# Kernel optimization log

Measured on AMD Instinct MI355X. Metric: run time of the kernel, lower is better.

The kernel has to match this reference:

```python
import jax, jax.numpy as jnp
import numpy as np

NUM_CODES = 4096
EMBED_DIM = 64
BETA = 0.25


def setup_inputs() -> dict:
    key = jax.random.key(0)
    k1, k2 = jax.random.split(key)
    z = jax.random.normal(k1, (8, EMBED_DIM, 64, 64), dtype=jnp.float32)
    weight = jax.random.normal(k2, (NUM_CODES, EMBED_DIM), dtype=jnp.float32)
    return {"z": z, "weight": weight}


def reference(z, weight):
    # z: [B, C, H, W] -> [B, H, W, C]
    z_bhwc = jnp.moveaxis(z, 1, -1)
    z_flat = z_bhwc.reshape(-1, EMBED_DIM)  # [N, d]

    # squared-euclidean distances: ||z||^2 + ||w||^2 - 2 z.w  -> [N, num_codes]
    distance = (
        jnp.sum(z_flat ** 2, axis=1, keepdims=True)
        + jnp.sum(weight ** 2, axis=1)
        - 2.0 * jnp.einsum('bd,nd->bn', z_flat, weight)
    )
    encoding_indices = jnp.argmin(distance, axis=1)  # [N]

    # codebook lookup (gather)
    z_q = weight[encoding_indices].reshape(z_bhwc.shape)  # [B, H, W, C]

    encodings = jax.nn.one_hot(encoding_indices, NUM_CODES, dtype=z.dtype)  # [N, num_codes]
    avg_probs = jnp.mean(encodings, axis=0)
    tiny = 1e-10  # max(1e-10, finfo(fp32).tiny)
    perplexity = jnp.exp(-jnp.sum(avg_probs * jnp.log(avg_probs + tiny)))

    # commitment loss (z_q detached) — eval path, no EMA state update
    loss = BETA * jnp.mean((jax.lax.stop_gradient(z_q) - z_bhwc) ** 2)

    # straight-through estimator
    z_q = z_bhwc + jax.lax.stop_gradient(z_q - z_bhwc)
    z_q = jnp.moveaxis(z_q, -1, 1)  # back to [B, C, H, W]

    return z_q, loss, perplexity, encodings, encoding_indices
```

## Files before the change

### kernel.cpp

```cpp
#include <hip/hip_runtime.h>
#include <math.h>
#include <float.h>

#define ZQ_OFF   0
#define LOSS_OFF 2097152
#define PERP_OFF 2097153
#define ENC_OFF  2097154
#define IDX_OFF  136314882ULL
#define BETA     0.25f


__global__ void vq_wnorm(const float* __restrict__ w, float* __restrict__ wnorm) {
    int c = blockIdx.x * 256 + threadIdx.x;
    const float4* w4 = (const float4*)(w + ((size_t)c << 6));
    float s = 0.f;
    #pragma unroll
    for (int k = 0; k < 16; ++k) { float4 v = w4[k]; s += v.x*v.x + v.y*v.y + v.z*v.z + v.w*v.w; }
    wnorm[c] = s;
}

__global__ __launch_bounds__(256, 2) void vq_main(
    const float* __restrict__ z, const float* __restrict__ w,
    const float* __restrict__ wnorm, float* __restrict__ out,
    float* __restrict__ loss_ws, int* __restrict__ ticket, int* __restrict__ hist)
{
    __shared__ float zD[64][64];
    __shared__ float wl[256 * 36];
    __shared__ int   s_widx[64];
    __shared__ int   s_flag;

    const int tx   = threadIdx.x;
    const int tcol = tx & 31;
    const int trow = tx >> 5;
    const int base = blockIdx.x * 64;
    const int bb   = base >> 12;
    const int hh   = (base & 4095) >> 6;

    #pragma unroll
    for (int j = 0; j < 4; ++j) {
        int f4 = j * 256 + tx;
        int d  = f4 >> 4, w4i = f4 & 15;
        float4 v = *(const float4*)(z + (((size_t)bb * 64 + d) * 64 + hh) * 64 + w4i * 4);
        *(float4*)&zD[d][w4i * 4] = v;
    }

    float best[8]; int bidx[8];
    #pragma unroll
    for (int i = 0; i < 8; ++i) { best[i] = FLT_MAX; bidx[i] = 0; }

    float* enc = out + ENC_OFF;

    for (int ch = 0; ch < 16; ++ch) {
        const int cbase = ch << 8;
        float wn[8];
        #pragma unroll
        for (int k = 0; k < 8; ++k) wn[k] = wnorm[cbase + tcol + 32 * k];

        float acc[8][8];
        #pragma unroll
        for (int i = 0; i < 8; ++i)
            #pragma unroll
            for (int k = 0; k < 8; ++k) acc[i][k] = 0.f;

        #pragma unroll
        for (int s = 0; s < 2; ++s) {
            __syncthreads();
            #pragma unroll
            for (int j = 0; j < 8; ++j) {
                int f4 = j * 256 + tx;
                int c  = f4 >> 3, q = f4 & 7;
                float4 v = ((const float4*)w)[(size_t)(cbase + c) * 16 + s * 8 + q];
                *(float4*)&wl[c * 36 + q * 4] = v;
            }
            #pragma unroll
            for (int j = 0; j < 16; ++j) {
                int f2 = ((ch * 2 + s) * 16 + j) * 256 + tx;
                int r  = f2 >> 11, c2 = f2 & 2047;
                *((float2*)(enc + ((size_t)(base + r) << 12)) + c2) = make_float2(0.f, 0.f);
            }
            __syncthreads();

            #pragma unroll
            for (int dg = 0; dg < 8; ++dg) {
                const int d0 = s * 32 + dg * 4;
                float4 zv0[4], zv1[4];
                #pragma unroll
                for (int e = 0; e < 4; ++e) {
                    zv0[e] = *(const float4*)&zD[d0 + e][trow * 8];
                    zv1[e] = *(const float4*)&zD[d0 + e][trow * 8 + 4];
                }
                float4 wv[8];
                #pragma unroll
                for (int k = 0; k < 8; ++k)
                    wv[k] = *(const float4*)&wl[(tcol + 32 * k) * 36 + dg * 4];
                #pragma unroll
                for (int k = 0; k < 8; ++k) {
                    #pragma unroll
                    for (int e = 0; e < 4; ++e) {
                        const float wf = (e == 0) ? wv[k].x : (e == 1) ? wv[k].y
                                        : (e == 2) ? wv[k].z : wv[k].w;
                        acc[0][k] = fmaf(zv0[e].x, wf, acc[0][k]);
                        acc[1][k] = fmaf(zv0[e].y, wf, acc[1][k]);
                        acc[2][k] = fmaf(zv0[e].z, wf, acc[2][k]);
                        acc[3][k] = fmaf(zv0[e].w, wf, acc[3][k]);
                        acc[4][k] = fmaf(zv1[e].x, wf, acc[4][k]);
                        acc[5][k] = fmaf(zv1[e].y, wf, acc[5][k]);
                        acc[6][k] = fmaf(zv1[e].z, wf, acc[6][k]);
                        acc[7][k] = fmaf(zv1[e].w, wf, acc[7][k]);
                    }
                }
            }
        }

        #pragma unroll
        for (int i = 0; i < 8; ++i) {
            #pragma unroll
            for (int k = 0; k < 8; ++k) {
                float sc = fmaf(-2.f, acc[i][k], wn[k]);
                if (sc < best[i]) { best[i] = sc; bidx[i] = cbase + tcol + 32 * k; }
            }
        }
    }

    __syncthreads();
    float2* red = (float2*)wl;
    #pragma unroll
    for (int i = 0; i < 8; ++i)
        red[(trow * 8 + i) * 32 + tcol] = make_float2(best[i], __int_as_float(bidx[i]));
    __syncthreads();

    if (tx < 64) {
        float b = FLT_MAX; int bi = 0x7fffffff;
        for (int c = 0; c < 32; ++c) {
            float2 v = red[tx * 32 + c];
            int vi = __float_as_int(v.y);
            if (v.x < b || (v.x == b && vi < bi)) { b = v.x; bi = vi; }
        }
        s_widx[tx] = bi;
        out[IDX_OFF + (size_t)(base + tx)] = (float)bi;
        atomicAdd(&hist[bi], 1);
        enc[((size_t)(base + tx) << 12) + bi] = 1.0f;
    }
    __syncthreads();

    {
        const int row = tx & 63;
        const int dg  = tx >> 6;
        const int wi  = s_widx[row];
        const float* qrow = w + ((size_t)wi << 6);
        float lsum = 0.f;
        #pragma unroll
        for (int dd = 0; dd < 16; ++dd) {
            int d = dg * 16 + dd;
            float q  = qrow[d];
            float zv = zD[d][row];
            float diff = q - zv;
            lsum += diff * diff;
            out[ZQ_OFF + (((size_t)bb * 64 + d) * 64 + hh) * 64 + row] = zv + (q - zv);
        }
        #pragma unroll
        for (int off = 32; off > 0; off >>= 1) lsum += __shfl_down(lsum, off, 64);
        if ((tx & 63) == 0) atomicAdd(loss_ws, lsum);
    }

    __syncthreads();
    if (tx == 0) {
        __threadfence();
        int old = atomicAdd(ticket, 1);
        s_flag = (old == 511) ? 1 : 0;
    }
    __syncthreads();
    if (s_flag) {
        __threadfence();
        float s = 0.f;
        #pragma unroll
        for (int j = 0; j < 16; ++j) {
            int c = tx + j * 256;
            int cnt = atomicAdd(&hist[c], 0);
            float p = (float)cnt * (1.f / 32768.f);
            s += p * logf(p + 1e-10f);
        }
        float* fr = wl;
        fr[tx] = s;
        __syncthreads();
        for (int off = 128; off > 0; off >>= 1) {
            if (tx < off) fr[tx] += fr[tx + off];
            __syncthreads();
        }
        if (tx == 0) {
            out[LOSS_OFF] = BETA * atomicAdd(loss_ws, 0.f) / 2097152.f;
            out[PERP_OFF] = expf(-fr[0]);
        }
    }
}

extern "C" void kernel_launch(void* const* d_in, const int* in_sizes, int n_in,
                              void* d_out, int out_size, void* d_ws, size_t ws_size,
                              hipStream_t stream)
{
    const float* z = (const float*)d_in[0];
    const float* w = (const float*)d_in[1];
    float* out     = (float*)d_out;
    float* loss_ws = (float*)d_ws;
    int*   ticket  = (int*)((char*)d_ws + 4);
    int*   hist    = (int*)((char*)d_ws + 16);
    float* wnorm   = (float*)((char*)d_ws + 16400);

    hipMemsetAsync(d_ws, 0, 16 + 4096 * sizeof(int), stream);
    vq_wnorm<<<16, 256, 0, stream>>>(w, wnorm);
    vq_main<<<512, 256, 0, stream>>>(z, w, wnorm, out, loss_ws, ticket, hist);
}
```

Before: 742.2 us.

## Register-prefetch next codebook tile and flatten chunk loop in VQ kernel

Flattens the 16x2 chunk loop into a single 32-step loop. Each step prefetches the next codebook half-tile from global memory into registers while the current tile is computed, so global load latency overlaps with the FMA work. The shared-memory row stride drops from 36 to 34 floats, and weight values are read from LDS one float4 at a time inside the k loop, which lowers register pressure. The costs are 32 extra registers for the prefetch buffer and a changed LDS bank pattern; the stride of 34 breaks 16-byte alignment for float4 accesses on odd rows.

```diff
diff --git a/kernel.cpp b/kernel.cpp
--- a/kernel.cpp
+++ b/kernel.cpp
@@ -9,6 +9,8 @@
 #define IDX_OFF  136314882ULL
 #define BETA     0.25f
 
+#define WSTRIDE  34
+
 
 __global__ void vq_wnorm(const float* __restrict__ w, float* __restrict__ wnorm) {
     int c = blockIdx.x * 256 + threadIdx.x;
@@ -18,6 +20,16 @@
     for (int k = 0; k < 16; ++k) { float4 v = w4[k]; s += v.x*v.x + v.y*v.y + v.z*v.z + v.w*v.w; }
     wnorm[c] = s;
 }
+
+#define FMA8(ZA, ZB, WF, K) \
+    acc[0][K] = fmaf((ZA).x, (WF), acc[0][K]); \
+    acc[1][K] = fmaf((ZA).y, (WF), acc[1][K]); \
+    acc[2][K] = fmaf((ZA).z, (WF), acc[2][K]); \
+    acc[3][K] = fmaf((ZA).w, (WF), acc[3][K]); \
+    acc[4][K] = fmaf((ZB).x, (WF), acc[4][K]); \
+    acc[5][K] = fmaf((ZB).y, (WF), acc[5][K]); \
+    acc[6][K] = fmaf((ZB).z, (WF), acc[6][K]); \
+    acc[7][K] = fmaf((ZB).w, (WF), acc[7][K]);
 
 __global__ __launch_bounds__(256, 2) void vq_main(
     const float* __restrict__ z, const float* __restrict__ w,
@@ -25,7 +37,7 @@
     float* __restrict__ loss_ws, int* __restrict__ ticket, int* __restrict__ hist)
 {
     __shared__ float zD[64][64];
-    __shared__ float wl[256 * 36];
+    __shared__ float wl[256 * WSTRIDE];
     __shared__ int   s_widx[64];
     __shared__ int   s_flag;
 
@@ -50,74 +62,78 @@
 
     float* enc = out + ENC_OFF;
 
-    for (int ch = 0; ch < 16; ++ch) {
+    const int stc = tx >> 3;
+    const int stq = tx & 7;
+    float4 pw[8];
+    #pragma unroll
+    for (int j = 0; j < 8; ++j)
+        pw[j] = ((const float4*)w)[(size_t)(j * 32 + stc) * 16 + stq];
+
+    float acc[8][8];
+    float wn[8];
+
+    for (int p = 0; p < 32; ++p) {
+        const int ch = p >> 1, s = p & 1;
         const int cbase = ch << 8;
-        float wn[8];
-        #pragma unroll
-        for (int k = 0; k < 8; ++k) wn[k] = wnorm[cbase + tcol + 32 * k];
-
-        float acc[8][8];
-        #pragma unroll
-        for (int i = 0; i < 8; ++i)
-            #pragma unroll
-            for (int k = 0; k < 8; ++k) acc[i][k] = 0.f;
-
-        #pragma unroll
-        for (int s = 0; s < 2; ++s) {
-            __syncthreads();
-            #pragma unroll
-            for (int j = 0; j < 8; ++j) {
-                int f4 = j * 256 + tx;
-                int c  = f4 >> 3, q = f4 & 7;
-                float4 v = ((const float4*)w)[(size_t)(cbase + c) * 16 + s * 8 + q];
-                *(float4*)&wl[c * 36 + q * 4] = v;
+
+        __syncthreads();
+        #pragma unroll
+        for (int j = 0; j < 8; ++j)
+            *(float4*)&wl[(j * 32 + stc) * WSTRIDE + stq * 4] = pw[j];
+        __syncthreads();
+
+        {
+            const int pn = (p < 31) ? p + 1 : 31;
+            const int cbn = (pn >> 1) << 8, sn = pn & 1;
+            #pragma unroll
+            for (int j = 0; j < 8; ++j)
+                pw[j] = ((const float4*)w)[(size_t)(cbn + j * 32 + stc) * 16 + sn * 8 + stq];
+        }
+        #pragma unroll
+        for (int j = 0; j < 16; ++j) {
+            int f2 = (p * 16 + j) * 256 + tx;
+            int r  = f2 >> 11, c2 = f2 & 2047;
+            *((float2*)(enc + ((size_t)(base + r) << 12)) + c2) = make_float2(0.f, 0.f);
+        }
+
+        if (s == 0) {
+            #pragma unroll
+            for (int k = 0; k < 8; ++k) wn[k] = wnorm[cbase + tcol + 32 * k];
+            #pragma unroll
+            for (int i = 0; i < 8; ++i)
+                #pragma unroll
+                for (int k = 0; k < 8; ++k) acc[i][k] = 0.f;
+        }
+
+        #pragma unroll
+        for (int dg = 0; dg < 8; ++dg) {
+            const int d0 = s * 32 + dg * 4;
+            float4 za0 = *(const float4*)&zD[d0    ][trow * 8];
+            float4 zb0 = *(const float4*)&zD[d0    ][trow * 8 + 4];
+            float4 za1 = *(const float4*)&zD[d0 + 1][trow * 8];
+            float4 zb1 = *(const float4*)&zD[d0 + 1][trow * 8 + 4];
+            float4 za2 = *(const float4*)&zD[d0 + 2][trow * 8];
+            float4 zb2 = *(const float4*)&zD[d0 + 2][trow * 8 + 4];
+            float4 za3 = *(const float4*)&zD[d0 + 3][trow * 8];
+            float4 zb3 = *(const float4*)&zD[d0 + 3][trow * 8 + 4];
+            #pragma unroll
+            for (int k = 0; k < 8; ++k) {
+                float4 wv = *(const float4*)&wl[(tcol + 32 * k) * WSTRIDE + dg * 4];
+                FMA8(za0, zb0, wv.x, k);
+                FMA8(za1, zb1, wv.y, k);
+                FMA8(za2, zb2, wv.z, k);
+                FMA8(za3, zb3, wv.w, k);
             }
-            #pragma unroll
-            for (int j = 0; j < 16; ++j) {
-                int f2 = ((ch * 2 + s) * 16 + j) * 256 + tx;
-                int r  = f2 >> 11, c2 = f2 & 2047;
-                *((float2*)(enc + ((size_t)(base + r) << 12)) + c2) = make_float2(0.f, 0.f);
-            }
-            __syncthreads();
-
-            #pragma unroll
-            for (int dg = 0; dg < 8; ++dg) {
-                const int d0 = s * 32 + dg * 4;
-                float4 zv0[4], zv1[4];
-                #pragma unroll
-                for (int e = 0; e < 4; ++e) {
-                    zv0[e] = *(const float4*)&zD[d0 + e][trow * 8];
-                    zv1[e] = *(const float4*)&zD[d0 + e][trow * 8 + 4];
-                }
-                float4 wv[8];
-                #pragma unroll
-                for (int k = 0; k < 8; ++k)
-                    wv[k] = *(const float4*)&wl[(tcol + 32 * k) * 36 + dg * 4];
+        }
+
+        if (s == 1) {
+            #pragma unroll
+            for (int i = 0; i < 8; ++i) {
                 #pragma unroll
                 for (int k = 0; k < 8; ++k) {
-                    #pragma unroll
-                    for (int e = 0; e < 4; ++e) {
-                        const float wf = (e == 0) ? wv[k].x : (e == 1) ? wv[k].y
-                                        : (e == 2) ? wv[k].z : wv[k].w;
-                        acc[0][k] = fmaf(zv0[e].x, wf, acc[0][k]);
-                        acc[1][k] = fmaf(zv0[e].y, wf, acc[1][k]);
-                        acc[2][k] = fmaf(zv0[e].z, wf, acc[2][k]);
-                        acc[3][k] = fmaf(zv0[e].w, wf, acc[3][k]);
-                        acc[4][k] = fmaf(zv1[e].x, wf, acc[4][k]);
-                        acc[5][k] = fmaf(zv1[e].y, wf, acc[5][k]);
-                        acc[6][k] = fmaf(zv1[e].z, wf, acc[6][k]);
-                        acc[7][k] = fmaf(zv1[e].w, wf, acc[7][k]);
-                    }
+                    float scv = fmaf(-2.f, acc[i][k], wn[k]);
+                    if (scv < best[i]) { best[i] = scv; bidx[i] = cbase + tcol + 32 * k; }
                 }
-            }
-        }
-
-        #pragma unroll
-        for (int i = 0; i < 8; ++i) {
-            #pragma unroll
-            for (int k = 0; k < 8; ++k) {
-                float sc = fmaf(-2.f, acc[i][k], wn[k]);
-                if (sc < best[i]) { best[i] = sc; bidx[i] = cbase + tcol + 32 * k; }
             }
         }
     }
```

Result: slower. 851.9 us (+14.8%).
